# Kernel optimization log

Hardware: AMD Instinct MI355X
Metric: run time of the kernel (lower is better)

## Reference

```python
import jax, jax.numpy as jnp
import numpy as np

N_NODES = 100000
N_EDGES = 1600000
IN_F = 256
OUT_F = 128


def setup_inputs() -> dict:
    key = jax.random.key(0)
    k1, k2, k3, k4, k5, k6 = jax.random.split(key, 6)
    x = jax.random.normal(k1, (N_NODES, IN_F), dtype=jnp.float32)
    stdv = 1.0 / np.sqrt(OUT_F)
    weight = jax.random.uniform(k2, (IN_F, OUT_F), dtype=jnp.float32, minval=-stdv, maxval=stdv)
    bias = jax.random.uniform(k3, (OUT_F,), dtype=jnp.float32, minval=-stdv, maxval=stdv)
    edge_src = jax.random.randint(k4, (N_EDGES,), 0, N_NODES, dtype=jnp.int32)
    edge_dst = jnp.sort(jax.random.randint(k5, (N_EDGES,), 0, N_NODES, dtype=jnp.int32))
    edge_val = jax.random.uniform(k6, (N_EDGES,), dtype=jnp.float32)
    return {"x": x, "weight": weight, "bias": bias,
            "edge_src": edge_src, "edge_dst": edge_dst, "edge_val": edge_val}


def reference(x, weight, bias, edge_src, edge_dst, edge_val):
    # support = X @ W   (dense GEMM, [N, out_f])
    support = x @ weight
    # output = A @ support, A sparse COO: out[dst] += val * support[src]
    msgs = support[edge_src] * edge_val[:, None]          # [E, out_f]
    output = jax.ops.segment_sum(msgs, edge_dst, num_segments=N_NODES,
                                 indices_are_sorted=True)  # [N, out_f]
    return jnp.tanh(output + bias)
```

## Files before the change

### kernel.cpp

```cpp
#include <hip/hip_runtime.h>
#include <hip/hip_bf16.h>

typedef _Float16 f16;
typedef f16 f16x8 __attribute__((ext_vector_type(8)));
typedef f16 f16x2 __attribute__((ext_vector_type(2)));
typedef float f32x4 __attribute__((ext_vector_type(4)));

#define IN_F 256
#define OUT_F 128

__global__ __launch_bounds__(256) void prep_w(const float* __restrict__ W,
                                              f16* __restrict__ Wt) {
    int i = blockIdx.x * 256 + threadIdx.x;
    int k = i >> 7;
    int n = i & 127;
    Wt[n * IN_F + k] = (f16)W[i];
}

__global__ __launch_bounds__(256) void seg_bounds(const int* __restrict__ dst,
                                                  int* __restrict__ rs,
                                                  int* __restrict__ re, int E) {
    int i = blockIdx.x * 256 + threadIdx.x;
    if (i >= E) return;
    int d = dst[i];
    if (i == 0 || dst[i - 1] != d) rs[d] = i;
    if (i == E - 1 || dst[i + 1] != d) re[d] = i + 1;
}

__global__ __launch_bounds__(256) void gemm_xw(const float* __restrict__ X,
                                               const f16* __restrict__ Wt,
                                               f16* __restrict__ S, int M) {
    const int w = threadIdx.x >> 6;
    const int l = threadIdx.x & 63;
    const int r = l & 15;
    const int khi = l >> 4;
    const int wm = w >> 1, wn = w & 1;
    const int mbase = blockIdx.x * 128 + wm * 64;
    const int nbase = wn * 64;

    f32x4 acc[4][4] = {};

    #pragma unroll
    for (int ks = 0; ks < 8; ++ks) {
        const int k0 = ks * 32 + khi * 8;
        f16x8 a[4], b[4];
        #pragma unroll
        for (int m = 0; m < 4; ++m) {
            int row = mbase + m * 16 + r;
            row = row < M ? row : M - 1;
            const float4* p = (const float4*)(X + (size_t)row * IN_F + k0);
            float4 x0 = p[0], x1 = p[1];
            a[m][0] = (f16)x0.x; a[m][1] = (f16)x0.y;
            a[m][2] = (f16)x0.z; a[m][3] = (f16)x0.w;
            a[m][4] = (f16)x1.x; a[m][5] = (f16)x1.y;
            a[m][6] = (f16)x1.z; a[m][7] = (f16)x1.w;
        }
        #pragma unroll
        for (int n = 0; n < 4; ++n) {
            int col = nbase + n * 16 + r;
            b[n] = *(const f16x8*)(Wt + (size_t)col * IN_F + k0);
        }
        #pragma unroll
        for (int m = 0; m < 4; ++m)
            #pragma unroll
            for (int n = 0; n < 4; ++n)
                acc[m][n] = __builtin_amdgcn_mfma_f32_16x16x32_f16(a[m], b[n], acc[m][n], 0, 0, 0);
    }

    #pragma unroll
    for (int m = 0; m < 4; ++m) {
        int row0 = mbase + m * 16 + khi * 4;
        #pragma unroll
        for (int i = 0; i < 4; ++i) {
            int row = row0 + i;
            if (row < M) {
                #pragma unroll
                for (int n = 0; n < 4; ++n)
                    S[(size_t)row * OUT_F + nbase + n * 16 + r] = (f16)acc[m][n][i];
            }
        }
    }
}

__global__ __launch_bounds__(256) void aggregate(const f16* __restrict__ S,
                                                 const int* __restrict__ rs,
                                                 const int* __restrict__ re,
                                                 const int* __restrict__ esrc,
                                                 const float* __restrict__ eval,
                                                 const float* __restrict__ bias,
                                                 float* __restrict__ out, int N) {
    const int wave = threadIdx.x >> 6;
    const int lane = threadIdx.x & 63;
    const int node = blockIdx.x * 4 + wave;
    if (node >= N) return;

    const int g = lane >> 4;
    const int p = lane & 15;

    const int s = rs[node];
    const int e = re[node];

    float acc[8] = {};

    for (int base = s; base < e; base += 16) {
        int   se[4];
        float ve[4];
        #pragma unroll
        for (int j = 0; j < 4; ++j) {
            int ei  = base + j * 4 + g;
            int eic = min(ei, e - 1);
            se[j] = esrc[eic];
            ve[j] = eval[eic];
            if (ei >= e) ve[j] = 0.f;
        }
        f16x8 h[4];
        #pragma unroll
        for (int j = 0; j < 4; ++j)
            h[j] = *(const f16x8*)(S + (size_t)se[j] * OUT_F + p * 8);
        #pragma unroll
        for (int j = 0; j < 4; ++j)
            #pragma unroll
            for (int q = 0; q < 8; ++q)
                acc[q] += ve[j] * (float)h[j][q];
    }

    #pragma unroll
    for (int q = 0; q < 8; ++q) {
        acc[q] += __shfl_xor(acc[q], 16);
        acc[q] += __shfl_xor(acc[q], 32);
    }

    if (lane < 32) {
        const int half = lane >> 4;
        const int f0 = 8 * p + 4 * half;
        float4 bb = *(const float4*)(bias + f0);
        float4 o;
        o.x = tanhf(acc[4 * half + 0] + bb.x);
        o.y = tanhf(acc[4 * half + 1] + bb.y);
        o.z = tanhf(acc[4 * half + 2] + bb.z);
        o.w = tanhf(acc[4 * half + 3] + bb.w);
        *(float4*)(out + (size_t)node * OUT_F + f0) = o;
    }
}

extern "C" void kernel_launch(void* const* d_in, const int* in_sizes, int n_in,
                              void* d_out, int out_size, void* d_ws, size_t ws_size,
                              hipStream_t stream) {
    const float* X    = (const float*)d_in[0];
    const float* W    = (const float*)d_in[1];
    const float* bias = (const float*)d_in[2];
    const int*   esrc = (const int*)d_in[3];
    const int*   edst = (const int*)d_in[4];
    const float* eval = (const float*)d_in[5];
    float* out = (float*)d_out;

    const int N = in_sizes[0] / IN_F;
    const int E = in_sizes[3];

    char* ws = (char*)d_ws;
    f16* Wt = (f16*)ws;
    f16* S  = (f16*)(ws + 65536);
    int* rs = (int*)(ws + 65536 + (size_t)N * OUT_F * 2);
    int* re = rs + N;

    hipMemsetAsync(rs, 0, 2 * (size_t)N * sizeof(int), stream);
    prep_w<<<(IN_F * OUT_F) / 256, 256, 0, stream>>>(W, Wt);
    seg_bounds<<<(E + 255) / 256, 256, 0, stream>>>(edst, rs, re, E);
    gemm_xw<<<(N + 127) / 128, 256, 0, stream>>>(X, Wt, S, N);
    aggregate<<<(N + 3) / 4, 256, 0, stream>>>(S, rs, re, esrc, eval, bias, out, N);
}
```

Measured before the change: 132.0 us.

## Stage X tiles through double-buffered swizzled LDS in GEMM with coalesced loads

```diff
diff --git a/kernel.cpp b/kernel.cpp
--- a/kernel.cpp
+++ b/kernel.cpp
@@ -3,11 +3,13 @@
 
 typedef _Float16 f16;
 typedef f16 f16x8 __attribute__((ext_vector_type(8)));
+typedef f16 f16x4 __attribute__((ext_vector_type(4)));
 typedef f16 f16x2 __attribute__((ext_vector_type(2)));
 typedef float f32x4 __attribute__((ext_vector_type(4)));
 
 #define IN_F 256
 #define OUT_F 128
+#define BK 64
 
 __global__ __launch_bounds__(256) void prep_w(const float* __restrict__ W,
                                               f16* __restrict__ Wt) {
@@ -30,46 +32,81 @@
 __global__ __launch_bounds__(256) void gemm_xw(const float* __restrict__ X,
                                                const f16* __restrict__ Wt,
                                                f16* __restrict__ S, int M) {
-    const int w = threadIdx.x >> 6;
-    const int l = threadIdx.x & 63;
-    const int r = l & 15;
+    __shared__ f16 sx[2][128 * BK] __attribute__((aligned(16)));
+
+    const int w   = threadIdx.x >> 6;
+    const int l   = threadIdx.x & 63;
+    const int r   = l & 15;
     const int khi = l >> 4;
     const int wm = w >> 1, wn = w & 1;
-    const int mbase = blockIdx.x * 128 + wm * 64;
+    const int brow  = blockIdx.x * 128;
+    const int mbase = wm * 64;
     const int nbase = wn * 64;
 
+    const int srow = w * 32 + (l >> 4);
+    const int scol = (l & 15) * 4;
+
     f32x4 acc[4][4] = {};
-
-    #pragma unroll
-    for (int ks = 0; ks < 8; ++ks) {
-        const int k0 = ks * 32 + khi * 8;
-        f16x8 a[4], b[4];
-        #pragma unroll
-        for (int m = 0; m < 4; ++m) {
-            int row = mbase + m * 16 + r;
-            row = row < M ? row : M - 1;
-            const float4* p = (const float4*)(X + (size_t)row * IN_F + k0);
-            float4 x0 = p[0], x1 = p[1];
-            a[m][0] = (f16)x0.x; a[m][1] = (f16)x0.y;
-            a[m][2] = (f16)x0.z; a[m][3] = (f16)x0.w;
-            a[m][4] = (f16)x1.x; a[m][5] = (f16)x1.y;
-            a[m][6] = (f16)x1.z; a[m][7] = (f16)x1.w;
-        }
-        #pragma unroll
-        for (int n = 0; n < 4; ++n) {
-            int col = nbase + n * 16 + r;
-            b[n] = *(const f16x8*)(Wt + (size_t)col * IN_F + k0);
-        }
-        #pragma unroll
-        for (int m = 0; m < 4; ++m)
+    float4 xv[8];
+
+    #pragma unroll
+    for (int j = 0; j < 8; ++j) {
+        int rloc = srow + j * 4;
+        int rg = brow + rloc; rg = rg < M ? rg : M - 1;
+        xv[j] = *(const float4*)(X + (size_t)rg * IN_F + scol);
+    }
+    #pragma unroll
+    for (int j = 0; j < 8; ++j) {
+        int rloc = srow + j * 4;
+        f16x4 hv = { (f16)xv[j].x, (f16)xv[j].y, (f16)xv[j].z, (f16)xv[j].w };
+        *(f16x4*)&sx[0][rloc * BK + (scol ^ ((rloc & 7) << 3))] = hv;
+    }
+    __syncthreads();
+
+    #pragma unroll
+    for (int t = 0; t < 4; ++t) {
+        if (t < 3) {
+            const int k0 = (t + 1) * BK;
+            #pragma unroll
+            for (int j = 0; j < 8; ++j) {
+                int rloc = srow + j * 4;
+                int rg = brow + rloc; rg = rg < M ? rg : M - 1;
+                xv[j] = *(const float4*)(X + (size_t)rg * IN_F + k0 + scol);
+            }
+        }
+        #pragma unroll
+        for (int kk = 0; kk < 2; ++kk) {
+            f16x8 a[4], b[4];
+            const int sidx = (kk * 32 + khi * 8) ^ ((r & 7) << 3);
+            #pragma unroll
+            for (int m = 0; m < 4; ++m) {
+                int arow = mbase + m * 16 + r;
+                a[m] = *(const f16x8*)&sx[t & 1][arow * BK + sidx];
+            }
+            const int kg = t * BK + kk * 32 + khi * 8;
             #pragma unroll
             for (int n = 0; n < 4; ++n)
-                acc[m][n] = __builtin_amdgcn_mfma_f32_16x16x32_f16(a[m], b[n], acc[m][n], 0, 0, 0);
+                b[n] = *(const f16x8*)(Wt + (size_t)(nbase + n * 16 + r) * IN_F + kg);
+            #pragma unroll
+            for (int m = 0; m < 4; ++m)
+                #pragma unroll
+                for (int n = 0; n < 4; ++n)
+                    acc[m][n] = __builtin_amdgcn_mfma_f32_16x16x32_f16(a[m], b[n], acc[m][n], 0, 0, 0);
+        }
+        if (t < 3) {
+            #pragma unroll
+            for (int j = 0; j < 8; ++j) {
+                int rloc = srow + j * 4;
+                f16x4 hv = { (f16)xv[j].x, (f16)xv[j].y, (f16)xv[j].z, (f16)xv[j].w };
+                *(f16x4*)&sx[(t + 1) & 1][rloc * BK + (scol ^ ((rloc & 7) << 3))] = hv;
+            }
+        }
+        __syncthreads();
     }
 
     #pragma unroll
     for (int m = 0; m < 4; ++m) {
-        int row0 = mbase + m * 16 + khi * 4;
+        int row0 = brow + mbase + m * 16 + khi * 4;
         #pragma unroll
         for (int i = 0; i < 4; ++i) {
             int row = row0 + i;
```

Measured after the change: 114.4 us. 13.3% less time.
